# Kernel optimization log

Measured on AMD Instinct MI355X. Metric: run time of the kernel, lower is better.

The kernel has to match this reference:

```python
import jax, jax.numpy as jnp
import numpy as np
from jax import lax

DECAY = 0.1
THRESH = 0.5
LENS = 1.0
D_IN = 2 * 34 * 34  # 2312
HID = 800
NC = 10

@jax.custom_vjp
def act_fun(x):
    return (x > THRESH).astype(x.dtype)

def _act_fwd(x):
    return act_fun(x), x

def _act_bwd(x, g):
    p = jax.nn.sigmoid((x - THRESH) / LENS)
    return (g * p * (1.0 - p) / LENS,)

act_fun.defvjp(_act_fwd, _act_bwd)


def setup_inputs() -> dict:
    key = jax.random.key(0)
    ks = jax.random.split(key, 8)
    B, T = 128, 300
    inp = jax.random.uniform(ks[0], (B, 2, 34, 34, 50), dtype=jnp.float32)
    X = jnp.zeros((B, 2, 34, 34, T), dtype=jnp.float32)
    idx = jax.random.randint(ks[1], (B,), 0, T - 50)
    W1 = jax.random.normal(ks[2], (HID, D_IN), dtype=jnp.float32) * 0.02
    b1 = jnp.zeros((HID,), dtype=jnp.float32)
    W2 = jax.random.normal(ks[3], (NC, HID), dtype=jnp.float32) * 0.03
    b2 = jnp.zeros((NC,), dtype=jnp.float32)
    Wc = jax.random.uniform(ks[4], (1, HID + 4), dtype=jnp.float32)  # ctrl init U(0,1)
    bc = jax.random.uniform(ks[5], (1,), dtype=jnp.float32)
    return {"input": inp, "X": X, "idx": idx, "W1": W1, "b1": b1,
            "W2": W2, "b2": b2, "Wc": Wc, "bc": bc}


def _paste(Xi, clip_i, idx_i):
    # X[i, :, :, :, idx:idx+50] = input[i].view(2,34,34,50)
    return lax.dynamic_update_slice(Xi, clip_i, (0, 0, 0, idx_i))


def reference(input, X, idx, W1, b1, W2, b2, Wc, bc):
    B = X.shape[0]
    T = X.shape[-1]
    X = jax.vmap(_paste)(X, input, idx.astype(jnp.int32))
    xs = jnp.moveaxis(X.reshape(B, D_IN, T), -1, 0)  # [T, B, D_IN]

    t = jnp.arange(T)
    freqs = jnp.stack([
        jnp.ones(T), (t % 2 == 0).astype(jnp.float32),
        (t % 10 == 0).astype(jnp.float32), (t % 100 == 0).astype(jnp.float32),
    ], axis=1).astype(X.dtype)  # [T, 4]
    is_first = (t == 0)

    f32 = X.dtype
    carry0 = (
        jnp.zeros((B, HID), f32), jnp.zeros((B, HID), f32),   # h1_mem, h1_spike
        jnp.zeros((B, NC), f32), jnp.zeros((B, NC), f32),     # h2_mem, h2_spike
        jnp.zeros((B, 1), f32), jnp.zeros((B, 1), f32),       # c_mem, c_spike
        jnp.ones((B, 1), f32), jnp.zeros((B, NC), f32),       # bgt, h2_sumspike
    )

    def step(carry, inps):
        h1m, h1s, h2m, h2s, cm, cs, bgt, sum2 = carry
        x, fq, first = inps
        x_a = jnp.where(first, x, x * cs)
        bgt = jnp.where(cs == 1.0, bgt + 1.0, bgt)
        h1m = h1m * DECAY * (1.0 - h1s) + x_a @ W1.T + b1
        h1s = act_fun(h1m)
        h2m = h2m * DECAY * (1.0 - h2s) + h1s @ W2.T + b2
        h2s = act_fun(h2m)
        c_in = jnp.concatenate(
            [lax.stop_gradient(h1s), jnp.broadcast_to(fq, (B, 4))], axis=1)
        cm = cm * 0.1 * (1.0 - cs) + c_in @ Wc.T + bc
        cs = act_fun(cm)
        sum2 = sum2 + h2s
        return (h1m, h1s, h2m, h2s, cm, cs, bgt, sum2), None

    carry, _ = lax.scan(step, carry0, (xs, freqs, is_first))
    bgt, sum2 = carry[6], carry[7]
    rate = sum2 / bgt
    return rate, X
```

## Files before the change

kernel.cpp:

```cpp
#include <hip/hip_runtime.h>

#define D_IN 2312
#define HID  800
#define NCLS 10
#define BATCH 128
#define TSTEPS 300
#define WIN  50

#define MT 64
#define NT 32
#define BKK 16
#define NTM 100
#define NTN 25
#define GEMM_BLOCKS (NTM * NTN)
#define PASTE_BLOCKS 2048
#define BLK 128
#define TOTQ (BATCH * D_IN * (TSTEPS / 4))

__global__ __launch_bounds__(BLK) void fused_kernel(
    const float* __restrict__ inp,
    const float* __restrict__ W1,
    const int*   __restrict__ idx,
    float*       __restrict__ P,
    float*       __restrict__ outX)
{
  __shared__ float As[BKK][MT];
  __shared__ float Bs[BKK][NT + 4];

  int t  = threadIdx.x;
  int bx = blockIdx.x;

  if (bx < GEMM_BLOCKS) {
    int nt = bx / NTM;
    int mt = bx - nt * NTM;
    int m0 = mt * MT, n0 = nt * NT;

    int am = t & 63;
    int ah = t >> 6;
    int r  = m0 + am;
    int bb = r / 50, ss = r - bb * 50;
    const float* aptr = inp + (size_t)bb * (D_IN * WIN) + ss;

    int bn = t >> 4;
    int bk = t & 15;

    int l  = t & 63;
    int lm = l & 7;
    int ln = l >> 3;
    int tm = ah * 32 + lm * 4;
    int tn = ln * 4;

    float aN[8], bN[4];
#pragma unroll
    for (int q = 0; q < 8; ++q) aN[q] = aptr[(ah * 8 + q) * WIN];
#pragma unroll
    for (int p = 0; p < 4; ++p)
      bN[p] = W1[(size_t)(n0 + bn + 8 * p) * D_IN + bk];

    float acc[4][4] = {};

    for (int k0 = 0; k0 < D_IN; k0 += BKK) {
#pragma unroll
      for (int q = 0; q < 8; ++q) As[ah * 8 + q][am] = aN[q];
#pragma unroll
      for (int p = 0; p < 4; ++p) Bs[bk][bn + 8 * p] = bN[p];
      __syncthreads();

      int kn0 = k0 + BKK;
      if (kn0 < D_IN) {
#pragma unroll
        for (int q = 0; q < 8; ++q) {
          int kk = kn0 + ah * 8 + q;
          aN[q] = (kk < D_IN) ? aptr[kk * WIN] : 0.f;
        }
#pragma unroll
        for (int p = 0; p < 4; ++p) {
          int kk = kn0 + bk;
          bN[p] = (kk < D_IN) ? W1[(size_t)(n0 + bn + 8 * p) * D_IN + kk] : 0.f;
        }
      }

#pragma unroll
      for (int kk = 0; kk < BKK; ++kk) {
        float4 A0 = *(const float4*)&As[kk][tm];
        float4 B0 = *(const float4*)&Bs[kk][tn];
        float av[4] = {A0.x, A0.y, A0.z, A0.w};
        float bv[4] = {B0.x, B0.y, B0.z, B0.w};
#pragma unroll
        for (int i = 0; i < 4; ++i)
#pragma unroll
          for (int j = 0; j < 4; ++j)
            acc[i][j] += av[i] * bv[j];
      }
      __syncthreads();
    }

#pragma unroll
    for (int i = 0; i < 4; ++i) {
      int row = m0 + tm + i;
      *(float4*)&P[(size_t)row * HID + n0 + tn] =
          make_float4(acc[i][0], acc[i][1], acc[i][2], acc[i][3]);
    }
  } else {
    int tid = (bx - GEMM_BLOCKS) * BLK + t;
    const int stride = PASTE_BLOCKS * BLK;
    for (int i = tid; i < TOTQ; i += stride) {
      int q  = i % 75;
      int rd = i / 75;
      int b  = rd / D_IN;
      int d  = rd - b * D_IN;
      int ib = idx[b];
      const float* ip = inp + (size_t)b * (D_IN * WIN) + (size_t)d * WIN;
      int t0 = q * 4;
      float v[4];
#pragma unroll
      for (int e = 0; e < 4; ++e) {
        unsigned w = (unsigned)(t0 + e - ib);
        v[e] = (w < (unsigned)WIN) ? ip[w] : 0.f;
      }
      *(float4*)&outX[(size_t)rd * TSTEPS + t0] = make_float4(v[0], v[1], v[2], v[3]);
    }
  }
}

__global__ __launch_bounds__(64, 1) void recur_kernel(
    const float* __restrict__ P,
    const float* __restrict__ W2,
    const float* __restrict__ b2,
    const float* __restrict__ Wc,
    const float* __restrict__ bc,
    const float* __restrict__ b1,
    const int*   __restrict__ idx,
    float*       __restrict__ out)
{
  __shared__ float sW2row[NCLS][832];

  int L = threadIdx.x;
  int b = blockIdx.x;

#pragma unroll
  for (int c = 0; c < NCLS; ++c)
    for (int base = 0; base < 832; base += 64) {
      int j = base + L;
      sW2row[c][j] = (j < HID) ? W2[c * HID + j] : 0.f;
    }

  int myidx = idx[b];
  const float* Pb = P + (size_t)b * WIN * HID;

  float m[13], b1r[13], wcr[13];
  unsigned smask = 0;
#pragma unroll
  for (int rr = 0; rr < 13; ++rr) {
    int j = L + 64 * rr;
    m[rr]   = 0.f;
    b1r[rr] = (j < HID) ? b1[j] : 0.f;
    wcr[rr] = (j < HID) ? Wc[j] : 0.f;
  }

  float cm = 0.f, cs = 0.f, bgt = 1.f;
  float bc0 = bc[0];
  float wf0 = Wc[HID], wf1 = Wc[HID + 1], wf2 = Wc[HID + 2], wf3 = Wc[HID + 3];

  float h2m[10], h2s[10], sum2[10], b2r[10];
#pragma unroll
  for (int c = 0; c < NCLS; ++c) { h2m[c] = 0.f; h2s[c] = 0.f; sum2[c] = 0.f; b2r[c] = b2[c]; }

  __syncthreads();

  float cur[13];
  {
    unsigned w0 = (unsigned)(0 - myidx);
    if (w0 < (unsigned)WIN) {
      const float* Pr = Pb + (size_t)w0 * HID;
#pragma unroll
      for (int rr = 0; rr < 13; ++rr) {
        int j = L + 64 * rr;
        cur[rr] = (j < HID) ? Pr[j] : 0.f;
      }
    } else {
#pragma unroll
      for (int rr = 0; rr < 13; ++rr) cur[rr] = 0.f;
    }
  }

  for (int step = 0; step < TSTEPS; ++step) {
    float gate = (step == 0) ? 1.f : cs;

    float nxt[13];
    {
      unsigned wn = (unsigned)(step + 1 - myidx);
      if (wn < (unsigned)WIN) {
        const float* Pr = Pb + (size_t)wn * HID;
#pragma unroll
        for (int rr = 0; rr < 13; ++rr) {
          int j = L + 64 * rr;
          nxt[rr] = (j < HID) ? Pr[j] : 0.f;
        }
      } else {
#pragma unroll
        for (int rr = 0; rr < 13; ++rr) nxt[rr] = 0.f;
      }
    }

    unsigned nmask = 0;
#pragma unroll
    for (int rr = 0; rr < 13; ++rr) {
      float mprev = ((smask >> rr) & 1u) ? 0.f : m[rr] * 0.1f;
      float mv = mprev + cur[rr] * gate + b1r[rr];
      m[rr] = mv;
      nmask |= (mv > 0.5f) ? (1u << rr) : 0u;
    }
    smask = nmask;

    unsigned long long ball = __ballot(smask != 0u);

    float ctrl = 0.f;
    float dot[10];
#pragma unroll
    for (int c = 0; c < NCLS; ++c) dot[c] = 0.f;

    if (ball) {
      float cacc = 0.f;
#pragma unroll
      for (int rr = 0; rr < 13; ++rr) {
        float f = (float)((smask >> rr) & 1u);
        cacc = fmaf(f, wcr[rr], cacc);
      }
      cacc += __shfl_xor(cacc, 1);
      cacc += __shfl_xor(cacc, 2);
      cacc += __shfl_xor(cacc, 4);
      cacc += __shfl_xor(cacc, 8);
      cacc += __shfl_xor(cacc, 16);
      cacc += __shfl_xor(cacc, 32);
      ctrl = cacc;

#pragma unroll
      for (int rr = 0; rr < 13; ++rr) {
        float f = (float)((smask >> rr) & 1u);
        int j = L + 64 * rr;
#pragma unroll
        for (int c = 0; c < NCLS; ++c)
          dot[c] = fmaf(f, sW2row[c][j], dot[c]);
      }
#pragma unroll
      for (int c = 0; c < NCLS; ++c) {
        float v = dot[c];
        v += __shfl_xor(v, 1);
        v += __shfl_xor(v, 2);
        v += __shfl_xor(v, 4);
        v += __shfl_xor(v, 8);
        v += __shfl_xor(v, 16);
        v += __shfl_xor(v, 32);
        dot[c] = v;
      }
    }

    bgt += (cs == 1.f) ? 1.f : 0.f;
    float fq = wf0;
    if ((step & 1) == 0)   fq += wf1;
    if (step % 10 == 0)    fq += wf2;
    if (step % 100 == 0)   fq += wf3;
    float cv = (cs != 0.f ? 0.f : cm * 0.1f) + ctrl + fq + bc0;
    cm = cv;
    cs = (cv > 0.5f) ? 1.f : 0.f;

#pragma unroll
    for (int c = 0; c < NCLS; ++c) {
      float v = (h2s[c] != 0.f ? 0.f : h2m[c] * 0.1f) + dot[c] + b2r[c];
      h2m[c] = v;
      h2s[c] = (v > 0.5f) ? 1.f : 0.f;
      sum2[c] += h2s[c];
    }

#pragma unroll
    for (int rr = 0; rr < 13; ++rr) cur[rr] = nxt[rr];
  }

  if (L == 0) {
#pragma unroll
    for (int c = 0; c < NCLS; ++c) out[b * NCLS + c] = sum2[c] / bgt;
  }
}

extern "C" void kernel_launch(void* const* d_in, const int* in_sizes, int n_in,
                              void* d_out, int out_size, void* d_ws, size_t ws_size,
                              hipStream_t stream) {
  const float* inp = (const float*)d_in[0];
  const int*   idx = (const int*)d_in[2];
  const float* W1  = (const float*)d_in[3];
  const float* b1  = (const float*)d_in[4];
  const float* W2  = (const float*)d_in[5];
  const float* b2  = (const float*)d_in[6];
  const float* Wc  = (const float*)d_in[7];
  const float* bc  = (const float*)d_in[8];

  float* out = (float*)d_out;
  float* P   = (float*)d_ws;

  fused_kernel<<<GEMM_BLOCKS + PASTE_BLOCKS, BLK, 0, stream>>>(
      inp, W1, idx, P, out + BATCH * NCLS);

  recur_kernel<<<BATCH, 64, 0, stream>>>(P, W2, b2, Wc, bc, b1, idx, out);
}
```

Baseline: 1.123 ms.

## Double GEMM M-tile to 128 with 8x4 microtile, nontemporal paste stores

The GEMM M-tile grows from 64 to 128 rows, giving each thread an 8x4 accumulator microtile. Each A element is now reused across more outputs and there are half as many blocks. The block index order changes so adjacent blocks share the same M tile, and a fast path drops bounds checks on the prefetch loads for full K tiles. The paste loop now writes X with nontemporal vector stores to cut cache pollution. The cost is higher register pressure from the launch-bounds hint of 4 and fewer GEMM blocks to spread across the GPU.

```diff
diff --git a/kernel.cpp b/kernel.cpp
--- a/kernel.cpp
+++ b/kernel.cpp
@@ -7,17 +7,19 @@
 #define TSTEPS 300
 #define WIN  50
 
-#define MT 64
+#define MT 128
 #define NT 32
 #define BKK 16
-#define NTM 100
+#define NTM 50
 #define NTN 25
 #define GEMM_BLOCKS (NTM * NTN)
 #define PASTE_BLOCKS 2048
 #define BLK 128
 #define TOTQ (BATCH * D_IN * (TSTEPS / 4))
 
-__global__ __launch_bounds__(BLK) void fused_kernel(
+typedef float nfloat4 __attribute__((ext_vector_type(4)));
+
+__global__ __launch_bounds__(BLK, 4) void fused_kernel(
     const float* __restrict__ inp,
     const float* __restrict__ W1,
     const int*   __restrict__ idx,
@@ -31,12 +33,11 @@
   int bx = blockIdx.x;
 
   if (bx < GEMM_BLOCKS) {
-    int nt = bx / NTM;
-    int mt = bx - nt * NTM;
+    int mt = bx / NTN;
+    int nt = bx - mt * NTN;
     int m0 = mt * MT, n0 = nt * NT;
 
-    int am = t & 63;
-    int ah = t >> 6;
+    int am = t;
     int r  = m0 + am;
     int bb = r / 50, ss = r - bb * 50;
     const float* aptr = inp + (size_t)bb * (D_IN * WIN) + ss;
@@ -44,33 +45,40 @@
     int bn = t >> 4;
     int bk = t & 15;
 
+    int ah = t >> 6;
     int l  = t & 63;
     int lm = l & 7;
     int ln = l >> 3;
-    int tm = ah * 32 + lm * 4;
+    int tm = ah * 64 + lm * 8;
     int tn = ln * 4;
 
-    float aN[8], bN[4];
-#pragma unroll
-    for (int q = 0; q < 8; ++q) aN[q] = aptr[(ah * 8 + q) * WIN];
+    float aN[16], bN[4];
+#pragma unroll
+    for (int q = 0; q < 16; ++q) aN[q] = aptr[q * WIN];
 #pragma unroll
     for (int p = 0; p < 4; ++p)
       bN[p] = W1[(size_t)(n0 + bn + 8 * p) * D_IN + bk];
 
-    float acc[4][4] = {};
+    float acc[8][4] = {};
 
     for (int k0 = 0; k0 < D_IN; k0 += BKK) {
 #pragma unroll
-      for (int q = 0; q < 8; ++q) As[ah * 8 + q][am] = aN[q];
+      for (int q = 0; q < 16; ++q) As[q][am] = aN[q];
 #pragma unroll
       for (int p = 0; p < 4; ++p) Bs[bk][bn + 8 * p] = bN[p];
       __syncthreads();
 
       int kn0 = k0 + BKK;
-      if (kn0 < D_IN) {
-#pragma unroll
-        for (int q = 0; q < 8; ++q) {
-          int kk = kn0 + ah * 8 + q;
+      if (kn0 + BKK <= D_IN) {
+#pragma unroll
+        for (int q = 0; q < 16; ++q) aN[q] = aptr[(kn0 + q) * WIN];
+#pragma unroll
+        for (int p = 0; p < 4; ++p)
+          bN[p] = W1[(size_t)(n0 + bn + 8 * p) * D_IN + kn0 + bk];
+      } else if (kn0 < D_IN) {
+#pragma unroll
+        for (int q = 0; q < 16; ++q) {
+          int kk = kn0 + q;
           aN[q] = (kk < D_IN) ? aptr[kk * WIN] : 0.f;
         }
 #pragma unroll
@@ -83,11 +91,12 @@
 #pragma unroll
       for (int kk = 0; kk < BKK; ++kk) {
         float4 A0 = *(const float4*)&As[kk][tm];
+        float4 A1 = *(const float4*)&As[kk][tm + 4];
         float4 B0 = *(const float4*)&Bs[kk][tn];
-        float av[4] = {A0.x, A0.y, A0.z, A0.w};
+        float av[8] = {A0.x, A0.y, A0.z, A0.w, A1.x, A1.y, A1.z, A1.w};
         float bv[4] = {B0.x, B0.y, B0.z, B0.w};
 #pragma unroll
-        for (int i = 0; i < 4; ++i)
+        for (int i = 0; i < 8; ++i)
 #pragma unroll
           for (int j = 0; j < 4; ++j)
             acc[i][j] += av[i] * bv[j];
@@ -96,7 +105,7 @@
     }
 
 #pragma unroll
-    for (int i = 0; i < 4; ++i) {
+    for (int i = 0; i < 8; ++i) {
       int row = m0 + tm + i;
       *(float4*)&P[(size_t)row * HID + n0 + tn] =
           make_float4(acc[i][0], acc[i][1], acc[i][2], acc[i][3]);
@@ -112,13 +121,13 @@
       int ib = idx[b];
       const float* ip = inp + (size_t)b * (D_IN * WIN) + (size_t)d * WIN;
       int t0 = q * 4;
-      float v[4];
+      nfloat4 v;
 #pragma unroll
       for (int e = 0; e < 4; ++e) {
         unsigned w = (unsigned)(t0 + e - ib);
         v[e] = (w < (unsigned)WIN) ? ip[w] : 0.f;
       }
-      *(float4*)&outX[(size_t)rd * TSTEPS + t0] = make_float4(v[0], v[1], v[2], v[3]);
+      __builtin_nontemporal_store(v, (nfloat4*)&outX[(size_t)rd * TSTEPS + t0]);
     }
   }
 }
```

After: 1.659 ms. +47.7%, slower.
